# Optimization experiments

Hardware: AMD Instinct MI355X
Metric: run time of the kernel (lower is better)

Reference implementation:

```python
import jax, jax.numpy as jnp
import numpy as np

M, N, F = 8192, 4096, 1


def quat_to_rotmat(q):
    # q: [N,4] (w,x,y,z) -> [N,3,3]
    q = q / jnp.linalg.norm(q, axis=-1, keepdims=True)
    w, x, y, z = q[:, 0], q[:, 1], q[:, 2], q[:, 3]
    r00 = 1 - 2 * (y * y + z * z)
    r01 = 2 * (x * y - w * z)
    r02 = 2 * (x * z + w * y)
    r10 = 2 * (x * y + w * z)
    r11 = 1 - 2 * (x * x + z * z)
    r12 = 2 * (y * z - w * x)
    r20 = 2 * (x * z - w * y)
    r21 = 2 * (y * z + w * x)
    r22 = 1 - 2 * (x * x + y * y)
    R = jnp.stack([jnp.stack([r00, r01, r02], -1),
                   jnp.stack([r10, r11, r12], -1),
                   jnp.stack([r20, r21, r22], -1)], -2)
    return R


def setup_inputs() -> dict:
    key = jax.random.key(0)
    k1, k2, k3, k4, k5, k6 = jax.random.split(key, 6)
    points = jax.random.normal(k1, (M, 3), dtype=jnp.float32)
    xyz = jax.random.normal(k2, (N, 3), dtype=jnp.float32)
    scale_raw = jax.random.normal(k3, (N, 3), dtype=jnp.float32) * 0.5  # _scale param
    rotation_raw = jax.random.normal(k4, (N, 4), dtype=jnp.float32)     # _rotation param
    opacity_raw = jax.random.normal(k5, (N, 1), dtype=jnp.float32)      # _opacity param
    features = jax.random.normal(k6, (N, F), dtype=jnp.float32)         # _features param
    return {"points": points, "xyz": xyz, "scale_raw": scale_raw,
            "rotation_raw": rotation_raw, "opacity_raw": opacity_raw,
            "features": features}


def reference(points, xyz, scale_raw, rotation_raw, opacity_raw, features):
    scale = jnp.exp(scale_raw)                       # [N,3] activation
    R = quat_to_rotmat(rotation_raw)                 # [N,3,3]
    RS = R * scale[:, None, :]                       # R @ diag(scale)
    cov = jnp.einsum('nik,njk->nij', RS, RS)         # [N,3,3]
    cov_inv = jnp.linalg.inv(cov)                    # [N,3,3]
    diff = points[:, None, :] - xyz[None, :, :]      # [M,N,3]
    mahal = jnp.einsum('mni,nij,mnj->mn', diff, cov_inv, diff)  # [M,N]
    influence = jnp.exp(-0.5 * mahal)                # [M,N]
    opacity = jax.nn.sigmoid(opacity_raw)            # [N,1]
    weights = influence * opacity.T                  # [M,N]
    values = weights @ features                      # [M,F]
    return values, weights
```

## Files before the change

kernel.cpp:

```cpp
#include <hip/hip_runtime.h>


#define THREADS 256
#define JPT 4
#define CHUNKS 4
#define MPB 16
#define NN 4096
#define MM 8192

__global__ __launch_bounds__(THREADS, 2) void gauss_fused(
    const float* __restrict__ points,
    const float* __restrict__ xyz,
    const float* __restrict__ scale_raw,
    const float* __restrict__ rot_raw,
    const float* __restrict__ op_raw,
    const float* __restrict__ feat,
    float* __restrict__ values,
    float* __restrict__ weights) {
  const int t = threadIdx.x;
  const int mbase = blockIdx.x * MPB;

  float gx[CHUNKS][JPT], gy[CHUNKS][JPT], gz[CHUNKS][JPT];
  float i00[CHUNKS][JPT], i01[CHUNKS][JPT], i02[CHUNKS][JPT];
  float i11[CHUNKS][JPT], i12[CHUNKS][JPT], i22[CHUNKS][JPT];
  float lop[CHUNKS][JPT], gf[CHUNKS][JPT];

#pragma unroll
  for (int c = 0; c < CHUNKS; ++c) {
    const int nb = c * (NN / CHUNKS) + t * JPT;
    const float4* rot4 = (const float4*)(rot_raw + 4 * (size_t)nb);
    const float4 q0 = rot4[0], q1 = rot4[1], q2 = rot4[2], q3 = rot4[3];
    const float4* sc4 = (const float4*)(scale_raw + 3 * (size_t)nb);
    const float4 s0 = sc4[0], s1 = sc4[1], s2 = sc4[2];
    const float4* xy4 = (const float4*)(xyz + 3 * (size_t)nb);
    const float4 p0 = xy4[0], p1 = xy4[1], p2 = xy4[2];
    const float4 op4 = *(const float4*)(op_raw + nb);
    const float4 f4  = *(const float4*)(feat + nb);

    const float4 q[JPT] = {q0, q1, q2, q3};
    const float sxa[JPT] = {s0.x, s0.w, s1.z, s2.y};
    const float sya[JPT] = {s0.y, s1.x, s1.w, s2.z};
    const float sza[JPT] = {s0.z, s1.y, s2.x, s2.w};
    const float xxa[JPT] = {p0.x, p0.w, p1.z, p2.y};
    const float yya[JPT] = {p0.y, p1.x, p1.w, p2.z};
    const float zza[JPT] = {p0.z, p1.y, p2.x, p2.w};
    const float opa[JPT] = {op4.x, op4.y, op4.z, op4.w};
    const float fa[JPT]  = {f4.x, f4.y, f4.z, f4.w};

#pragma unroll
    for (int j = 0; j < JPT; ++j) {
      float qw = q[j].x, qx = q[j].y, qy = q[j].z, qz = q[j].w;
      const float inorm = rsqrtf(qw*qw + qx*qx + qy*qy + qz*qz);
      qw *= inorm; qx *= inorm; qy *= inorm; qz *= inorm;
      const float sx = __expf(sxa[j]);
      const float sy = __expf(sya[j]);
      const float sz = __expf(sza[j]);
      const float r00 = 1.f - 2.f*(qy*qy + qz*qz);
      const float r01 = 2.f*(qx*qy - qw*qz);
      const float r02 = 2.f*(qx*qz + qw*qy);
      const float r10 = 2.f*(qx*qy + qw*qz);
      const float r11 = 1.f - 2.f*(qx*qx + qz*qz);
      const float r12 = 2.f*(qy*qz - qw*qx);
      const float r20 = 2.f*(qx*qz - qw*qy);
      const float r21 = 2.f*(qy*qz + qw*qx);
      const float r22 = 1.f - 2.f*(qx*qx + qy*qy);
      const float a0 = r00*sx, a1 = r01*sy, a2 = r02*sz;
      const float b0 = r10*sx, b1 = r11*sy, b2 = r12*sz;
      const float c0 = r20*sx, c1 = r21*sy, c2 = r22*sz;
      const float c00 = a0*a0 + a1*a1 + a2*a2;
      const float c01 = a0*b0 + a1*b1 + a2*b2;
      const float c02 = a0*c0 + a1*c1 + a2*c2;
      const float c11 = b0*b0 + b1*b1 + b2*b2;
      const float c12 = b0*c0 + b1*c1 + b2*c2;
      const float c22 = c0*c0 + c1*c1 + c2*c2;
      const float m00 = c11*c22 - c12*c12;
      const float m01 = c02*c12 - c01*c22;
      const float m02 = c01*c12 - c02*c11;
      const float det = c00*m00 + c01*m01 + c02*m02;
      const float idet = 1.f / det;
      i00[c][j] = m00*idet;
      i01[c][j] = m01*idet;
      i02[c][j] = m02*idet;
      i11[c][j] = (c00*c22 - c02*c02)*idet;
      i12[c][j] = (c02*c01 - c00*c12)*idet;
      i22[c][j] = (c00*c11 - c01*c01)*idet;
      gx[c][j] = xxa[j]; gy[c][j] = yya[j]; gz[c][j] = zza[j];
      lop[c][j] = -__log2f(1.f + __expf(-opa[j]));
      gf[c][j] = fa[j];
    }
  }

  float vs[MPB];
  const int wv = t >> 6;
  __shared__ float part[MPB][THREADS / 64];

#pragma unroll 2
  for (int i = 0; i < MPB; ++i) {
    const int m = mbase + i;
    const float px = points[3*m+0];
    const float py = points[3*m+1];
    const float pz = points[3*m+2];
    float vsum = 0.f;
#pragma unroll
    for (int c = 0; c < CHUNKS; ++c) {
      float4 w;
#pragma unroll
      for (int j = 0; j < JPT; ++j) {
        const float dx = px - gx[c][j];
        const float dy = py - gy[c][j];
        const float dz = pz - gz[c][j];
        const float t0 = i00[c][j]*dx + i01[c][j]*dy + i02[c][j]*dz;
        const float t1 = i01[c][j]*dx + i11[c][j]*dy + i12[c][j]*dz;
        const float t2 = i02[c][j]*dx + i12[c][j]*dy + i22[c][j]*dz;
        const float mahal = dx*t0 + dy*t1 + dz*t2;
        const float wj = exp2f(fmaf(mahal, -0.72134752044448170f, lop[c][j]));
        (&w.x)[j] = wj;
        vsum = fmaf(wj, gf[c][j], vsum);
      }
      *(float4*)&weights[(size_t)m * NN + c * (NN / CHUNKS) + t * JPT] = w;
    }
    vs[i] = vsum;
  }

#pragma unroll
  for (int i = 0; i < MPB; ++i) {
#pragma unroll
    for (int off = 32; off >= 1; off >>= 1)
      vs[i] += __shfl_xor(vs[i], off, 64);
  }
  if ((t & 63) == 0) {
#pragma unroll
    for (int i = 0; i < MPB; ++i) part[i][wv] = vs[i];
  }
  __syncthreads();
  if (t < MPB) {
    values[mbase + t] = (part[t][0] + part[t][1]) + (part[t][2] + part[t][3]);
  }
}

extern "C" void kernel_launch(void* const* d_in, const int* in_sizes, int n_in,
                              void* d_out, int out_size, void* d_ws, size_t ws_size,
                              hipStream_t stream) {
  const float* points    = (const float*)d_in[0];
  const float* xyz       = (const float*)d_in[1];
  const float* scale_raw = (const float*)d_in[2];
  const float* rot_raw   = (const float*)d_in[3];
  const float* op_raw    = (const float*)d_in[4];
  const float* feat      = (const float*)d_in[5];

  float* values  = (float*)d_out;
  float* weights = (float*)d_out + MM;

  gauss_fused<<<MM / MPB, THREADS, 0, stream>>>(
      points, xyz, scale_raw, rot_raw, op_raw, feat, values, weights);
}
```

Before: 38.74 us.

## Expand Mahalanobis quadratic into precomputed polynomial coefficients and use nontemporal stores

Measured after the change: 34.46 us. 1.12x faster.

```diff
diff --git a/kernel.cpp b/kernel.cpp
--- a/kernel.cpp
+++ b/kernel.cpp
@@ -7,6 +7,8 @@
 #define MPB 16
 #define NN 4096
 #define MM 8192
+
+typedef float f32x4 __attribute__((ext_vector_type(4)));
 
 __global__ __launch_bounds__(THREADS, 2) void gauss_fused(
     const float* __restrict__ points,
@@ -20,10 +22,12 @@
   const int t = threadIdx.x;
   const int mbase = blockIdx.x * MPB;
 
-  float gx[CHUNKS][JPT], gy[CHUNKS][JPT], gz[CHUNKS][JPT];
-  float i00[CHUNKS][JPT], i01[CHUNKS][JPT], i02[CHUNKS][JPT];
-  float i11[CHUNKS][JPT], i12[CHUNKS][JPT], i22[CHUNKS][JPT];
-  float lop[CHUNKS][JPT], gf[CHUNKS][JPT];
+  float A00[CHUNKS][JPT], A01[CHUNKS][JPT], A02[CHUNKS][JPT];
+  float A11[CHUNKS][JPT], A12[CHUNKS][JPT], A22[CHUNKS][JPT];
+  float B0[CHUNKS][JPT], B1[CHUNKS][JPT], B2[CHUNKS][JPT];
+  float CC[CHUNKS][JPT], FF[CHUNKS][JPT];
+
+  const float k = -0.72134752044448170f;
 
 #pragma unroll
   for (int c = 0; c < CHUNKS; ++c) {
@@ -65,28 +69,42 @@
       const float r21 = 2.f*(qy*qz + qw*qx);
       const float r22 = 1.f - 2.f*(qx*qx + qy*qy);
       const float a0 = r00*sx, a1 = r01*sy, a2 = r02*sz;
-      const float b0 = r10*sx, b1 = r11*sy, b2 = r12*sz;
-      const float c0 = r20*sx, c1 = r21*sy, c2 = r22*sz;
+      const float b0_ = r10*sx, b1_ = r11*sy, b2_ = r12*sz;
+      const float c0_ = r20*sx, c1_ = r21*sy, c2_ = r22*sz;
       const float c00 = a0*a0 + a1*a1 + a2*a2;
-      const float c01 = a0*b0 + a1*b1 + a2*b2;
-      const float c02 = a0*c0 + a1*c1 + a2*c2;
-      const float c11 = b0*b0 + b1*b1 + b2*b2;
-      const float c12 = b0*c0 + b1*c1 + b2*c2;
-      const float c22 = c0*c0 + c1*c1 + c2*c2;
+      const float c01 = a0*b0_ + a1*b1_ + a2*b2_;
+      const float c02 = a0*c0_ + a1*c1_ + a2*c2_;
+      const float c11 = b0_*b0_ + b1_*b1_ + b2_*b2_;
+      const float c12 = b0_*c0_ + b1_*c1_ + b2_*c2_;
+      const float c22 = c0_*c0_ + c1_*c1_ + c2_*c2_;
       const float m00 = c11*c22 - c12*c12;
       const float m01 = c02*c12 - c01*c22;
       const float m02 = c01*c12 - c02*c11;
       const float det = c00*m00 + c01*m01 + c02*m02;
       const float idet = 1.f / det;
-      i00[c][j] = m00*idet;
-      i01[c][j] = m01*idet;
-      i02[c][j] = m02*idet;
-      i11[c][j] = (c00*c22 - c02*c02)*idet;
-      i12[c][j] = (c02*c01 - c00*c12)*idet;
-      i22[c][j] = (c00*c11 - c01*c01)*idet;
-      gx[c][j] = xxa[j]; gy[c][j] = yya[j]; gz[c][j] = zza[j];
-      lop[c][j] = -__log2f(1.f + __expf(-opa[j]));
-      gf[c][j] = fa[j];
+      const float i00 = m00*idet;
+      const float i01 = m01*idet;
+      const float i02 = m02*idet;
+      const float i11 = (c00*c22 - c02*c02)*idet;
+      const float i12 = (c02*c01 - c00*c12)*idet;
+      const float i22 = (c00*c11 - c01*c01)*idet;
+      const float gx = xxa[j], gy = yya[j], gz = zza[j];
+      const float w0 = i00*gx + i01*gy + i02*gz;
+      const float w1 = i01*gx + i11*gy + i12*gz;
+      const float w2 = i02*gx + i12*gy + i22*gz;
+      A00[c][j] = k * i00;
+      A11[c][j] = k * i11;
+      A22[c][j] = k * i22;
+      A01[c][j] = 2.f * k * i01;
+      A02[c][j] = 2.f * k * i02;
+      A12[c][j] = 2.f * k * i12;
+      B0[c][j] = -2.f * k * w0;
+      B1[c][j] = -2.f * k * w1;
+      B2[c][j] = -2.f * k * w2;
+      const float gIg = gx*w0 + gy*w1 + gz*w2;
+      const float lop = -__log2f(1.f + __expf(-opa[j]));
+      CC[c][j] = k * gIg + lop;
+      FF[c][j] = fa[j];
     }
   }
 
@@ -100,24 +118,30 @@
     const float px = points[3*m+0];
     const float py = points[3*m+1];
     const float pz = points[3*m+2];
+    const float pxx = px*px, pyy = py*py, pzz = pz*pz;
+    const float pxy = px*py, pxz = px*pz, pyz = py*pz;
     float vsum = 0.f;
 #pragma unroll
     for (int c = 0; c < CHUNKS; ++c) {
-      float4 w;
+      f32x4 w;
 #pragma unroll
       for (int j = 0; j < JPT; ++j) {
-        const float dx = px - gx[c][j];
-        const float dy = py - gy[c][j];
-        const float dz = pz - gz[c][j];
-        const float t0 = i00[c][j]*dx + i01[c][j]*dy + i02[c][j]*dz;
-        const float t1 = i01[c][j]*dx + i11[c][j]*dy + i12[c][j]*dz;
-        const float t2 = i02[c][j]*dx + i12[c][j]*dy + i22[c][j]*dz;
-        const float mahal = dx*t0 + dy*t1 + dz*t2;
-        const float wj = exp2f(fmaf(mahal, -0.72134752044448170f, lop[c][j]));
-        (&w.x)[j] = wj;
-        vsum = fmaf(wj, gf[c][j], vsum);
+        float arg = CC[c][j];
+        arg = fmaf(B2[c][j], pz, arg);
+        arg = fmaf(B1[c][j], py, arg);
+        arg = fmaf(B0[c][j], px, arg);
+        arg = fmaf(A12[c][j], pyz, arg);
+        arg = fmaf(A02[c][j], pxz, arg);
+        arg = fmaf(A01[c][j], pxy, arg);
+        arg = fmaf(A22[c][j], pzz, arg);
+        arg = fmaf(A11[c][j], pyy, arg);
+        arg = fmaf(A00[c][j], pxx, arg);
+        const float wj = __builtin_amdgcn_exp2f(arg);
+        w[j] = wj;
+        vsum = fmaf(wj, FF[c][j], vsum);
       }
-      *(float4*)&weights[(size_t)m * NN + c * (NN / CHUNKS) + t * JPT] = w;
+      __builtin_nontemporal_store(
+          w, (f32x4*)&weights[(size_t)m * NN + c * (NN / CHUNKS) + t * JPT]);
     }
     vs[i] = vsum;
   }
```

## Split into per-Gaussian precompute kernel and quadratic-form sweep kernel

Applied to the files above, without the earlier changes.

Result: faster. 33.38 us (-13.8%).

```diff
diff --git a/kernel.cpp b/kernel.cpp
--- a/kernel.cpp
+++ b/kernel.cpp
@@ -3,123 +3,137 @@
 
 #define THREADS 256
 #define JPT 4
-#define CHUNKS 4
-#define MPB 16
+#define MPB 8
 #define NN 4096
 #define MM 8192
+#define CHUNKS (NN / (THREADS * JPT))
+#define NCOEF 11
 
-__global__ __launch_bounds__(THREADS, 2) void gauss_fused(
+typedef float f32x4 __attribute__((ext_vector_type(4)));
+
+__global__ void gauss_precomp(const float* __restrict__ xyz,
+                              const float* __restrict__ scale_raw,
+                              const float* __restrict__ rot_raw,
+                              const float* __restrict__ op_raw,
+                              const float* __restrict__ feat,
+                              float* __restrict__ C, int N) {
+  const int n = blockIdx.x * blockDim.x + threadIdx.x;
+  if (n >= N) return;
+  const float k = -0.72134752044448170f;
+  float qw = rot_raw[4*n+0], qx = rot_raw[4*n+1], qy = rot_raw[4*n+2], qz = rot_raw[4*n+3];
+  const float inorm = rsqrtf(qw*qw + qx*qx + qy*qy + qz*qz);
+  qw *= inorm; qx *= inorm; qy *= inorm; qz *= inorm;
+  const float sx = __expf(scale_raw[3*n+0]);
+  const float sy = __expf(scale_raw[3*n+1]);
+  const float sz = __expf(scale_raw[3*n+2]);
+  const float r00 = 1.f - 2.f*(qy*qy + qz*qz);
+  const float r01 = 2.f*(qx*qy - qw*qz);
+  const float r02 = 2.f*(qx*qz + qw*qy);
+  const float r10 = 2.f*(qx*qy + qw*qz);
+  const float r11 = 1.f - 2.f*(qx*qx + qz*qz);
+  const float r12 = 2.f*(qy*qz - qw*qx);
+  const float r20 = 2.f*(qx*qz - qw*qy);
+  const float r21 = 2.f*(qy*qz + qw*qx);
+  const float r22 = 1.f - 2.f*(qx*qx + qy*qy);
+  const float a0 = r00*sx, a1 = r01*sy, a2 = r02*sz;
+  const float b0 = r10*sx, b1 = r11*sy, b2 = r12*sz;
+  const float c0 = r20*sx, c1 = r21*sy, c2 = r22*sz;
+  const float c00 = a0*a0 + a1*a1 + a2*a2;
+  const float c01 = a0*b0 + a1*b1 + a2*b2;
+  const float c02 = a0*c0 + a1*c1 + a2*c2;
+  const float c11 = b0*b0 + b1*b1 + b2*b2;
+  const float c12 = b0*c0 + b1*c1 + b2*c2;
+  const float c22 = c0*c0 + c1*c1 + c2*c2;
+  const float m00 = c11*c22 - c12*c12;
+  const float m01 = c02*c12 - c01*c22;
+  const float m02 = c01*c12 - c02*c11;
+  const float det = c00*m00 + c01*m01 + c02*m02;
+  const float idet = 1.f / det;
+  const float i00 = m00*idet;
+  const float i01 = m01*idet;
+  const float i02 = m02*idet;
+  const float i11 = (c00*c22 - c02*c02)*idet;
+  const float i12 = (c02*c01 - c00*c12)*idet;
+  const float i22 = (c00*c11 - c01*c01)*idet;
+  const float gx = xyz[3*n+0], gy = xyz[3*n+1], gz = xyz[3*n+2];
+  const float w0 = i00*gx + i01*gy + i02*gz;
+  const float w1 = i01*gx + i11*gy + i12*gz;
+  const float w2 = i02*gx + i12*gy + i22*gz;
+  const float gIg = gx*w0 + gy*w1 + gz*w2;
+  const float lop = -__log2f(1.f + __expf(-op_raw[n]));
+  C[0*NN + n] = k * i00;
+  C[1*NN + n] = k * i11;
+  C[2*NN + n] = k * i22;
+  C[3*NN + n] = 2.f * k * i01;
+  C[4*NN + n] = 2.f * k * i02;
+  C[5*NN + n] = 2.f * k * i12;
+  C[6*NN + n] = -2.f * k * w0;
+  C[7*NN + n] = -2.f * k * w1;
+  C[8*NN + n] = -2.f * k * w2;
+  C[9*NN + n] = k * gIg + lop;
+  C[10*NN + n] = feat[n];
+}
+
+__global__ __launch_bounds__(THREADS, 4) void gauss_sweep(
     const float* __restrict__ points,
-    const float* __restrict__ xyz,
-    const float* __restrict__ scale_raw,
-    const float* __restrict__ rot_raw,
-    const float* __restrict__ op_raw,
-    const float* __restrict__ feat,
+    const float* __restrict__ C,
     float* __restrict__ values,
     float* __restrict__ weights) {
   const int t = threadIdx.x;
   const int mbase = blockIdx.x * MPB;
 
-  float gx[CHUNKS][JPT], gy[CHUNKS][JPT], gz[CHUNKS][JPT];
-  float i00[CHUNKS][JPT], i01[CHUNKS][JPT], i02[CHUNKS][JPT];
-  float i11[CHUNKS][JPT], i12[CHUNKS][JPT], i22[CHUNKS][JPT];
-  float lop[CHUNKS][JPT], gf[CHUNKS][JPT];
+  __shared__ float spts[MPB * 3];
+  __shared__ float part[MPB][THREADS / 64];
+  if (t < MPB * 3) spts[t] = points[mbase * 3 + t];
+  __syncthreads();
+
+  float vs[MPB];
+#pragma unroll
+  for (int i = 0; i < MPB; ++i) vs[i] = 0.f;
 
 #pragma unroll
   for (int c = 0; c < CHUNKS; ++c) {
-    const int nb = c * (NN / CHUNKS) + t * JPT;
-    const float4* rot4 = (const float4*)(rot_raw + 4 * (size_t)nb);
-    const float4 q0 = rot4[0], q1 = rot4[1], q2 = rot4[2], q3 = rot4[3];
-    const float4* sc4 = (const float4*)(scale_raw + 3 * (size_t)nb);
-    const float4 s0 = sc4[0], s1 = sc4[1], s2 = sc4[2];
-    const float4* xy4 = (const float4*)(xyz + 3 * (size_t)nb);
-    const float4 p0 = xy4[0], p1 = xy4[1], p2 = xy4[2];
-    const float4 op4 = *(const float4*)(op_raw + nb);
-    const float4 f4  = *(const float4*)(feat + nb);
-
-    const float4 q[JPT] = {q0, q1, q2, q3};
-    const float sxa[JPT] = {s0.x, s0.w, s1.z, s2.y};
-    const float sya[JPT] = {s0.y, s1.x, s1.w, s2.z};
-    const float sza[JPT] = {s0.z, s1.y, s2.x, s2.w};
-    const float xxa[JPT] = {p0.x, p0.w, p1.z, p2.y};
-    const float yya[JPT] = {p0.y, p1.x, p1.w, p2.z};
-    const float zza[JPT] = {p0.z, p1.y, p2.x, p2.w};
-    const float opa[JPT] = {op4.x, op4.y, op4.z, op4.w};
-    const float fa[JPT]  = {f4.x, f4.y, f4.z, f4.w};
+    const int n0 = c * (THREADS * JPT) + t * JPT;
+    f32x4 A00 = *(const f32x4*)&C[0*NN + n0];
+    f32x4 A11 = *(const f32x4*)&C[1*NN + n0];
+    f32x4 A22 = *(const f32x4*)&C[2*NN + n0];
+    f32x4 A01 = *(const f32x4*)&C[3*NN + n0];
+    f32x4 A02 = *(const f32x4*)&C[4*NN + n0];
+    f32x4 A12 = *(const f32x4*)&C[5*NN + n0];
+    f32x4 B0  = *(const f32x4*)&C[6*NN + n0];
+    f32x4 B1  = *(const f32x4*)&C[7*NN + n0];
+    f32x4 B2  = *(const f32x4*)&C[8*NN + n0];
+    f32x4 CC  = *(const f32x4*)&C[9*NN + n0];
+    f32x4 FF  = *(const f32x4*)&C[10*NN + n0];
 
 #pragma unroll
-    for (int j = 0; j < JPT; ++j) {
-      float qw = q[j].x, qx = q[j].y, qy = q[j].z, qz = q[j].w;
-      const float inorm = rsqrtf(qw*qw + qx*qx + qy*qy + qz*qz);
-      qw *= inorm; qx *= inorm; qy *= inorm; qz *= inorm;
-      const float sx = __expf(sxa[j]);
-      const float sy = __expf(sya[j]);
-      const float sz = __expf(sza[j]);
-      const float r00 = 1.f - 2.f*(qy*qy + qz*qz);
-      const float r01 = 2.f*(qx*qy - qw*qz);
-      const float r02 = 2.f*(qx*qz + qw*qy);
-      const float r10 = 2.f*(qx*qy + qw*qz);
-      const float r11 = 1.f - 2.f*(qx*qx + qz*qz);
-      const float r12 = 2.f*(qy*qz - qw*qx);
-      const float r20 = 2.f*(qx*qz - qw*qy);
-      const float r21 = 2.f*(qy*qz + qw*qx);
-      const float r22 = 1.f - 2.f*(qx*qx + qy*qy);
-      const float a0 = r00*sx, a1 = r01*sy, a2 = r02*sz;
-      const float b0 = r10*sx, b1 = r11*sy, b2 = r12*sz;
-      const float c0 = r20*sx, c1 = r21*sy, c2 = r22*sz;
-      const float c00 = a0*a0 + a1*a1 + a2*a2;
-      const float c01 = a0*b0 + a1*b1 + a2*b2;
-      const float c02 = a0*c0 + a1*c1 + a2*c2;
-      const float c11 = b0*b0 + b1*b1 + b2*b2;
-      const float c12 = b0*c0 + b1*c1 + b2*c2;
-      const float c22 = c0*c0 + c1*c1 + c2*c2;
-      const float m00 = c11*c22 - c12*c12;
-      const float m01 = c02*c12 - c01*c22;
-      const float m02 = c01*c12 - c02*c11;
-      const float det = c00*m00 + c01*m01 + c02*m02;
-      const float idet = 1.f / det;
-      i00[c][j] = m00*idet;
-      i01[c][j] = m01*idet;
-      i02[c][j] = m02*idet;
-      i11[c][j] = (c00*c22 - c02*c02)*idet;
-      i12[c][j] = (c02*c01 - c00*c12)*idet;
-      i22[c][j] = (c00*c11 - c01*c01)*idet;
-      gx[c][j] = xxa[j]; gy[c][j] = yya[j]; gz[c][j] = zza[j];
-      lop[c][j] = -__log2f(1.f + __expf(-opa[j]));
-      gf[c][j] = fa[j];
-    }
-  }
-
-  float vs[MPB];
-  const int wv = t >> 6;
-  __shared__ float part[MPB][THREADS / 64];
-
-#pragma unroll 2
-  for (int i = 0; i < MPB; ++i) {
-    const int m = mbase + i;
-    const float px = points[3*m+0];
-    const float py = points[3*m+1];
-    const float pz = points[3*m+2];
-    float vsum = 0.f;
-#pragma unroll
-    for (int c = 0; c < CHUNKS; ++c) {
-      float4 w;
+    for (int i = 0; i < MPB; ++i) {
+      const float px = spts[3*i+0];
+      const float py = spts[3*i+1];
+      const float pz = spts[3*i+2];
+      const float pxx = px*px, pyy = py*py, pzz = pz*pz;
+      const float pxy = px*py, pxz = px*pz, pyz = py*pz;
+      f32x4 w;
+      float vsum = vs[i];
 #pragma unroll
       for (int j = 0; j < JPT; ++j) {
-        const float dx = px - gx[c][j];
-        const float dy = py - gy[c][j];
-        const float dz = pz - gz[c][j];
-        const float t0 = i00[c][j]*dx + i01[c][j]*dy + i02[c][j]*dz;
-        const float t1 = i01[c][j]*dx + i11[c][j]*dy + i12[c][j]*dz;
-        const float t2 = i02[c][j]*dx + i12[c][j]*dy + i22[c][j]*dz;
-        const float mahal = dx*t0 + dy*t1 + dz*t2;
-        const float wj = exp2f(fmaf(mahal, -0.72134752044448170f, lop[c][j]));
-        (&w.x)[j] = wj;
-        vsum = fmaf(wj, gf[c][j], vsum);
+        float arg = CC[j];
+        arg = fmaf(B2[j], pz, arg);
+        arg = fmaf(B1[j], py, arg);
+        arg = fmaf(B0[j], px, arg);
+        arg = fmaf(A12[j], pyz, arg);
+        arg = fmaf(A02[j], pxz, arg);
+        arg = fmaf(A01[j], pxy, arg);
+        arg = fmaf(A22[j], pzz, arg);
+        arg = fmaf(A11[j], pyy, arg);
+        arg = fmaf(A00[j], pxx, arg);
+        const float wj = __builtin_amdgcn_exp2f(arg);
+        w[j] = wj;
+        vsum = fmaf(wj, FF[j], vsum);
       }
-      *(float4*)&weights[(size_t)m * NN + c * (NN / CHUNKS) + t * JPT] = w;
+      vs[i] = vsum;
+      *(f32x4*)&weights[(size_t)(mbase + i) * NN + n0] = w;
     }
-    vs[i] = vsum;
   }
 
 #pragma unroll
@@ -128,6 +142,7 @@
     for (int off = 32; off >= 1; off >>= 1)
       vs[i] += __shfl_xor(vs[i], off, 64);
   }
+  const int wv = t >> 6;
   if ((t & 63) == 0) {
 #pragma unroll
     for (int i = 0; i < MPB; ++i) part[i][wv] = vs[i];
@@ -150,7 +165,10 @@
 
   float* values  = (float*)d_out;
   float* weights = (float*)d_out + MM;
+  float* C       = (float*)d_ws;
 
-  gauss_fused<<<MM / MPB, THREADS, 0, stream>>>(
-      points, xyz, scale_raw, rot_raw, op_raw, feat, values, weights);
+  gauss_precomp<<<(NN + THREADS - 1) / THREADS, THREADS, 0, stream>>>(
+      xyz, scale_raw, rot_raw, op_raw, feat, C, NN);
+
+  gauss_sweep<<<MM / MPB, THREADS, 0, stream>>>(points, C, values, weights);
 }
```
